# Optimization experiments

Measured on AMD Instinct MI355X. Metric: run time of the kernel, lower is better.

The kernel has to match this reference:

```python
import jax, jax.numpy as jnp
import numpy as np

N = 50000          # number of points
C = 64             # num_clusters (embedding width)
K_RAD = 32         # radius graph max_num_neighbors
K_KNN = 10         # knn graph k


def setup_inputs() -> dict:
    key = jax.random.key(0)
    ks = jax.random.split(key, 8)
    x0 = jax.random.normal(ks[0], (N, 3), jnp.float32)
    pos0 = jax.random.normal(ks[1], (N, 3), jnp.float32)
    # R0/t0 come from rigid_fitting in the original (external helper); use
    # orthonormal matrices from batched QR as realistic per-point rotations.
    A = jax.random.normal(ks[2], (N, 3, 3), jnp.float32)
    R0, _ = jnp.linalg.qr(A)
    t0 = jax.random.normal(ks[3], (N, 3), jnp.float32) * 0.1
    # pool1 k=1 assignment: point i -> cluster assign01[i]
    assign01 = jax.random.randint(ks[4], (N,), 0, C, dtype=jnp.int32)
    # radius graph edges (source, target): each point has K_RAD neighbors
    radius_src = jax.random.randint(ks[5], (N * K_RAD,), 0, N, dtype=jnp.int32)
    radius_dst = jnp.repeat(jnp.arange(N, dtype=jnp.int32), K_RAD)
    # knn-10 graph edges used by WeightedAvg
    knn_src = jax.random.randint(ks[6], (N * K_KNN,), 0, N, dtype=jnp.int32)
    knn_dst = jnp.repeat(jnp.arange(N, dtype=jnp.int32), K_KNN)
    return dict(x0=x0, pos0=pos0, R0=R0, t0=t0, assign01=assign01,
                radius_src=radius_src, radius_dst=radius_dst,
                knn_src=knn_src, knn_dst=knn_dst)


def _rigid_layer(xfeat, pos0, x0, R0, t0, src, dst):
    # RigidPropModule.message + max aggregation (nn=None, lin1: w=-1, b=0.01)
    Ri = R0[dst]                     # [E,3,3] target-side rotation
    ti = t0[dst]                     # [E,3]
    posj = pos0[src]                 # [E,3]
    xj = x0[src]                     # [E,3]
    pred = jnp.einsum('eij,ej->ei', Ri, posj) + ti
    d = jnp.sum((pred - xj) ** 2, axis=-1, keepdims=True)   # [E,1]
    w = jax.nn.sigmoid(-d + 0.01)
    msg = w * xfeat[src]             # [E,C]
    agg = jax.ops.segment_max(msg, dst, num_segments=xfeat.shape[0])
    # messages are non-negative; nodes with no edges get 0 (torch_scatter fill)
    return jnp.maximum(agg, 0.0)


def reference(x0, pos0, R0, t0, assign01, radius_src, radius_dst, knn_src, knn_dst):
    n = x0.shape[0]
    # scatter_add of one-hot cluster embeddings back to points
    emb = jnp.zeros((n, C), jnp.float32).at[jnp.arange(n), assign01].add(1.0)
    m1 = _rigid_layer(emb, pos0, x0, R0, t0, radius_src, radius_dst)
    m2 = _rigid_layer(m1, pos0, x0, R0, t0, radius_src, radius_dst)
    m3 = _rigid_layer(m2, pos0, x0, R0, t0, radius_src, radius_dst)
    m4 = _rigid_layer(m2, pos0, x0, R0, t0, radius_src, radius_dst)
    m5 = _rigid_layer(m2, pos0, x0, R0, t0, radius_src, radius_dst)
    msg = jnp.stack([m1.sum(-1), m2.sum(-1), m3.sum(-1),
                     m4.sum(-1), m5.sum(-1)], axis=-1)      # [N,5]
    # predictor: Linear(5,1) with w=ones, b=-17, then sigmoid
    conf = jax.nn.sigmoid(msg.sum(-1, keepdims=True) - 17.0)  # [N,1]
    # WeightedAvg over knn edges: out[t] = sum_s conf[s]*val[s] / sum_s conf[s]
    cw = conf[knn_src]                                       # [E,1]
    num_R = jax.ops.segment_sum(cw * R0.reshape(n, 9)[knn_src], knn_dst, num_segments=n)
    num_t = jax.ops.segment_sum(cw * t0[knn_src], knn_dst, num_segments=n)
    den = jax.ops.segment_sum(cw, knn_dst, num_segments=n) + 1e-8
    R_out = (num_R / den).reshape(n, 3, 3)
    t_out = num_t / den
    x_out = jnp.einsum('nij,nj->ni', R_out, pos0) + t_out
    return x_out, R_out, t_out
```

## Files before the change

kernel.cpp:

```cpp
#include <hip/hip_runtime.h>
#include <hip/hip_fp16.h>
#include <math.h>

#define N_PTS 50000
#define C_DIM 64
#define K_RAD 32
#define K_KNN 10
#define E_RAD (N_PTS * K_RAD)

__device__ inline __half2 hmax2(__half2 a, __half2 b) {
    __half2 d;
    asm("v_pk_max_f16 %0, %1, %2" : "=v"(d) : "v"(a), "v"(b));
    return d;
}

__device__ inline __half2 shfl_xor_h2(__half2 v, int mask) {
    int i = *(int*)&v;
    int r = __shfl_xor(i, mask);
    return *(__half2*)&r;
}

__global__ void pack_tables_kernel(const float* __restrict__ pos0,
                                   const float* __restrict__ x0,
                                   const int* __restrict__ assign,
                                   float4* __restrict__ geo) {
    int i = blockIdx.x * blockDim.x + threadIdx.x;
    if (i >= N_PTS) return;
    geo[i * 2 + 0] = make_float4(pos0[3 * i], pos0[3 * i + 1], pos0[3 * i + 2], x0[3 * i]);
    geo[i * 2 + 1] = make_float4(x0[3 * i + 1], x0[3 * i + 2], __int_as_float(assign[i]), 0.0f);
}

__global__ void ew_layer1_kernel(const float4* __restrict__ geo,
                                 const float* __restrict__ R0,
                                 const float* __restrict__ t0,
                                 const int* __restrict__ src,
                                 unsigned int* __restrict__ packed,
                                 __half* __restrict__ m1,
                                 float* __restrict__ sum1,
                                 float4* __restrict__ rt4) {
    __shared__ int lm[16][C_DIM];
    __shared__ float ldsR[16 * 9];
    __shared__ float ldsT[16 * 3];
    int tid = threadIdx.x;
    int blk = blockIdx.x;
    ((int*)lm)[tid] = 0;
    ((int*)lm)[tid + 256] = 0;
    ((int*)lm)[tid + 512] = 0;
    ((int*)lm)[tid + 768] = 0;
    if (tid < 144) ldsR[tid] = R0[blk * 144 + tid];
    if (tid < 48) ldsT[tid] = t0[blk * 48 + tid];
    int nl = tid >> 4;
    int ng = blk * 16 + nl;
    int e0 = tid & 15, e1 = e0 + 16;
    int s0 = src[ng * K_RAD + e0];
    int s1 = src[ng * K_RAD + e1];
    float4 g0a = geo[s0 * 2 + 0];
    float4 g0b = geo[s0 * 2 + 1];
    float4 g1a = geo[s1 * 2 + 0];
    float4 g1b = geo[s1 * 2 + 1];
    __syncthreads();
    if (tid < 48) {
        int n = tid / 3, slot = tid % 3;
        const float* R = ldsR + n * 9;
        const float* T = ldsT + n * 3;
        float4 q;
        if (slot == 0) q = make_float4(R[0], R[1], R[2], R[3]);
        else if (slot == 1) q = make_float4(R[4], R[5], R[6], R[7]);
        else q = make_float4(R[8], T[0], T[1], T[2]);
        rt4[(blk * 16 + n) * 4 + slot] = q;
    }
    const float* R = ldsR + nl * 9;
    const float* T = ldsT + nl * 3;
    float r0 = R[0] * g0a.x + R[1] * g0a.y + R[2] * g0a.z + T[0] - g0a.w;
    float r1 = R[3] * g0a.x + R[4] * g0a.y + R[5] * g0a.z + T[1] - g0b.x;
    float r2 = R[6] * g0a.x + R[7] * g0a.y + R[8] * g0a.z + T[2] - g0b.y;
    float d0 = r0 * r0 + r1 * r1 + r2 * r2;
    float w0 = 1.0f / (1.0f + __expf(d0 - 0.01f));
    float u0 = R[0] * g1a.x + R[1] * g1a.y + R[2] * g1a.z + T[0] - g1a.w;
    float u1 = R[3] * g1a.x + R[4] * g1a.y + R[5] * g1a.z + T[1] - g1b.x;
    float u2 = R[6] * g1a.x + R[7] * g1a.y + R[8] * g1a.z + T[2] - g1b.y;
    float d1 = u0 * u0 + u1 * u1 + u2 * u2;
    float w1 = 1.0f / (1.0f + __expf(d1 - 0.01f));
    packed[ng * K_RAD + e0] =
        ((unsigned int)s0 << 16) | (unsigned int)__half_as_ushort(__float2half_rn(w0));
    packed[ng * K_RAD + e1] =
        ((unsigned int)s1 << 16) | (unsigned int)__half_as_ushort(__float2half_rn(w1));
    atomicMax(&lm[nl][__float_as_int(g0b.z)], __float_as_int(w0));
    atomicMax(&lm[nl][__float_as_int(g1b.z)], __float_as_int(w1));
    __syncthreads();
    int c0 = (tid & 15) * 4;
    float v0 = __int_as_float(lm[nl][c0 + 0]);
    float v1 = __int_as_float(lm[nl][c0 + 1]);
    float v2 = __int_as_float(lm[nl][c0 + 2]);
    float v3 = __int_as_float(lm[nl][c0 + 3]);
    __half2 h01 = __floats2half2_rn(v0, v1);
    __half2 h23 = __floats2half2_rn(v2, v3);
    uint2 uo = make_uint2(*(unsigned int*)&h01, *(unsigned int*)&h23);
    *(uint2*)(m1 + ng * C_DIM + c0) = uo;
    float s = v0 + v1 + v2 + v3;
    s += __shfl_down(s, 8);
    s += __shfl_down(s, 4);
    s += __shfl_down(s, 2);
    s += __shfl_down(s, 1);
    if ((tid & 15) == 0) sum1[ng] = s;
}

__global__ void layer_pk_kernel(const unsigned int* __restrict__ packed,
                                const __half* __restrict__ xin,
                                __half* __restrict__ xout,
                                float* __restrict__ sum_out) {
    int gid = blockIdx.x * blockDim.x + threadIdx.x;
    int lane = gid & 63;
    int node = (gid >> 6) * 2 + (lane >> 5);
    int eslot = (lane >> 3) & 3;
    int cpos = lane & 7;
    const uint4* pk4 = (const uint4*)(packed + node * K_RAD + eslot * 8);
    uint4 q0 = pk4[0], q1 = pk4[1];
    unsigned int pes[8] = {q0.x, q0.y, q0.z, q0.w, q1.x, q1.y, q1.z, q1.w};
    __half2 a0 = __float2half2_rn(0.0f), a1 = a0, a2 = a0, a3 = a0;
#pragma unroll
    for (int p = 0; p < 8; ++p) {
        unsigned int pe = pes[p];
        float4 f = *(const float4*)(xin + (pe >> 16) * C_DIM + cpos * 8);
        __half2* h = (__half2*)&f;
        __half2 w2 = __half2half2(__ushort_as_half((unsigned short)(pe & 0xffffu)));
        a0 = hmax2(a0, __hmul2(w2, h[0]));
        a1 = hmax2(a1, __hmul2(w2, h[1]));
        a2 = hmax2(a2, __hmul2(w2, h[2]));
        a3 = hmax2(a3, __hmul2(w2, h[3]));
    }
#pragma unroll
    for (int off = 8; off <= 16; off <<= 1) {
        a0 = hmax2(a0, shfl_xor_h2(a0, off));
        a1 = hmax2(a1, shfl_xor_h2(a1, off));
        a2 = hmax2(a2, shfl_xor_h2(a2, off));
        a3 = hmax2(a3, shfl_xor_h2(a3, off));
    }
    if (eslot == 0) {
        float4 o;
        __half2* oh = (__half2*)&o;
        oh[0] = a0; oh[1] = a1; oh[2] = a2; oh[3] = a3;
        ((float4*)(xout + node * C_DIM))[cpos] = o;
    }
    float2 v0 = __half22float2(a0), v1 = __half22float2(a1);
    float2 v2 = __half22float2(a2), v3 = __half22float2(a3);
    float s = v0.x + v0.y + v1.x + v1.y + v2.x + v2.y + v3.x + v3.y;
    s += __shfl_xor(s, 1);
    s += __shfl_xor(s, 2);
    s += __shfl_xor(s, 4);
    if ((lane & 31) == 0) sum_out[node] = s;
}

__global__ void layer3_conf_pk_kernel(const unsigned int* __restrict__ packed,
                                      const __half* __restrict__ xin,
                                      const float* __restrict__ sum1,
                                      const float* __restrict__ sum2,
                                      float* __restrict__ rt4f) {
    int gid = blockIdx.x * blockDim.x + threadIdx.x;
    int lane = gid & 63;
    int node = (gid >> 6) * 2 + (lane >> 5);
    int eslot = (lane >> 3) & 3;
    int cpos = lane & 7;
    const uint4* pk4 = (const uint4*)(packed + node * K_RAD + eslot * 8);
    uint4 q0 = pk4[0], q1 = pk4[1];
    unsigned int pes[8] = {q0.x, q0.y, q0.z, q0.w, q1.x, q1.y, q1.z, q1.w};
    __half2 a0 = __float2half2_rn(0.0f), a1 = a0, a2 = a0, a3 = a0;
#pragma unroll
    for (int p = 0; p < 8; ++p) {
        unsigned int pe = pes[p];
        float4 f = *(const float4*)(xin + (pe >> 16) * C_DIM + cpos * 8);
        __half2* h = (__half2*)&f;
        __half2 w2 = __half2half2(__ushort_as_half((unsigned short)(pe & 0xffffu)));
        a0 = hmax2(a0, __hmul2(w2, h[0]));
        a1 = hmax2(a1, __hmul2(w2, h[1]));
        a2 = hmax2(a2, __hmul2(w2, h[2]));
        a3 = hmax2(a3, __hmul2(w2, h[3]));
    }
#pragma unroll
    for (int off = 8; off <= 16; off <<= 1) {
        a0 = hmax2(a0, shfl_xor_h2(a0, off));
        a1 = hmax2(a1, shfl_xor_h2(a1, off));
        a2 = hmax2(a2, shfl_xor_h2(a2, off));
        a3 = hmax2(a3, shfl_xor_h2(a3, off));
    }
    float2 v0 = __half22float2(a0), v1 = __half22float2(a1);
    float2 v2 = __half22float2(a2), v3 = __half22float2(a3);
    float s = v0.x + v0.y + v1.x + v1.y + v2.x + v2.y + v3.x + v3.y;
    s += __shfl_xor(s, 1);
    s += __shfl_xor(s, 2);
    s += __shfl_xor(s, 4);
    if ((lane & 31) == 0) {
        float tot = sum1[node] + sum2[node] + 3.0f * s - 17.0f;
        rt4f[node * 16 + 12] = 1.0f / (1.0f + __expf(-tot));
    }
}

__global__ void wavg_kernel(const int* __restrict__ knn_src,
                            const float4* __restrict__ rt4,
                            const float* __restrict__ pos0,
                            float* __restrict__ out) {
    int gid = blockIdx.x * blockDim.x + threadIdx.x;
    int lane = gid & 63;
    int t = (gid >> 6) * 16 + (lane >> 2);
    int part = lane & 3;
    if (t >= N_PTS) return;
    float4 acc = make_float4(0.f, 0.f, 0.f, 0.f);
    for (int j = 0; j < K_KNN; ++j) {
        int s = knn_src[t * K_KNN + j];
        float4 q = rt4[s * 4 + part];
        float c = __shfl(q.x, lane | 3);
        if (part == 3) {
            acc.x += c;
        } else {
            acc.x += c * q.x; acc.y += c * q.y;
            acc.z += c * q.z; acc.w += c * q.w;
        }
    }
    float den = __shfl(acc.x, lane | 3) + 1e-8f;
    float inv = 1.0f / den;
    float4 sc = make_float4(acc.x * inv, acc.y * inv, acc.z * inv, acc.w * inv);
    int base = lane & ~3;
    float R3 = __shfl(sc.w, base + 0);
    float R6 = __shfl(sc.z, base + 1);
    float R7 = __shfl(sc.w, base + 1);
    float t0v = __shfl(sc.y, base + 2);
    float t1v = __shfl(sc.z, base + 2);
    float px = pos0[t * 3 + 0], py = pos0[t * 3 + 1], pz = pos0[t * 3 + 2];
    float* Rout = out + N_PTS * 3;
    float* tout = out + N_PTS * 12;
    if (part == 0) {
        out[t * 3 + 0] = sc.x * px + sc.y * py + sc.z * pz + t0v;
        Rout[t * 9 + 0] = sc.x; Rout[t * 9 + 1] = sc.y;
        Rout[t * 9 + 2] = sc.z; Rout[t * 9 + 3] = sc.w;
    } else if (part == 1) {
        out[t * 3 + 1] = R3 * px + sc.x * py + sc.y * pz + t1v;
        Rout[t * 9 + 4] = sc.x; Rout[t * 9 + 5] = sc.y;
        Rout[t * 9 + 6] = sc.z; Rout[t * 9 + 7] = sc.w;
    } else if (part == 2) {
        out[t * 3 + 2] = R6 * px + R7 * py + sc.x * pz + sc.w;
        Rout[t * 9 + 8] = sc.x;
        tout[t * 3 + 0] = sc.y; tout[t * 3 + 1] = sc.z; tout[t * 3 + 2] = sc.w;
    }
}

extern "C" void kernel_launch(void* const* d_in, const int* in_sizes, int n_in,
                              void* d_out, int out_size, void* d_ws, size_t ws_size,
                              hipStream_t stream) {
    const float* x0 = (const float*)d_in[0];
    const float* pos0 = (const float*)d_in[1];
    const float* R0 = (const float*)d_in[2];
    const float* t0 = (const float*)d_in[3];
    const int* assign01 = (const int*)d_in[4];
    const int* radius_src = (const int*)d_in[5];
    const int* knn_src = (const int*)d_in[7];

    char* ws = (char*)d_ws;
    unsigned int* packed = (unsigned int*)ws;
    __half* mA = (__half*)(ws + 6400000);
    __half* mB = (__half*)(ws + 12800000);
    float4* geo = (float4*)(ws + 19200000);
    float4* rt4 = (float4*)(ws + 20800000);
    float* sum1 = (float*)(ws + 24000000);
    float* sum2 = (float*)(ws + 24200000);
    float* out = (float*)d_out;

    pack_tables_kernel<<<(N_PTS + 255) / 256, 256, 0, stream>>>(
        pos0, x0, assign01, geo);

    ew_layer1_kernel<<<N_PTS / 16, 256, 0, stream>>>(
        geo, R0, t0, radius_src, packed, mA, sum1, rt4);

    layer_pk_kernel<<<N_PTS / 8, 256, 0, stream>>>(
        packed, mA, mB, sum2);

    layer3_conf_pk_kernel<<<N_PTS / 8, 256, 0, stream>>>(
        packed, mB, sum1, sum2, (float*)rt4);

    wavg_kernel<<<(N_PTS * 4 + 255) / 256, 256, 0, stream>>>(
        knn_src, rt4, pos0, out);
}
```

Before: 136.4 us.

## Add nontemporal loads/stores, batch gathers, fold sums into rt4, split knn across lanes

Streaming index, packed-edge and output accesses now use nontemporal loads and stores so they do not pollute cache. In the two gather layers, all eight neighbor feature loads are issued before any compute, exposing more memory-level parallelism. The per-node layer sums are written into spare slots of the rt4 table instead of separate arrays. The weighted-average kernel splits each node's ten knn neighbors across two lane groups and combines them with a shuffle. These changes raise register use and double the wavg thread count.

```diff
diff --git a/kernel.cpp b/kernel.cpp
--- a/kernel.cpp
+++ b/kernel.cpp
@@ -6,7 +6,9 @@
 #define C_DIM 64
 #define K_RAD 32
 #define K_KNN 10
-#define E_RAD (N_PTS * K_RAD)
+
+typedef unsigned int uv4 __attribute__((ext_vector_type(4)));
+typedef unsigned int uv2 __attribute__((ext_vector_type(2)));
 
 __device__ inline __half2 hmax2(__half2 a, __half2 b) {
     __half2 d;
@@ -36,11 +38,11 @@
                                  const int* __restrict__ src,
                                  unsigned int* __restrict__ packed,
                                  __half* __restrict__ m1,
-                                 float* __restrict__ sum1,
                                  float4* __restrict__ rt4) {
     __shared__ int lm[16][C_DIM];
     __shared__ float ldsR[16 * 9];
     __shared__ float ldsT[16 * 3];
+    float* rt4f = (float*)rt4;
     int tid = threadIdx.x;
     int blk = blockIdx.x;
     ((int*)lm)[tid] = 0;
@@ -52,8 +54,8 @@
     int nl = tid >> 4;
     int ng = blk * 16 + nl;
     int e0 = tid & 15, e1 = e0 + 16;
-    int s0 = src[ng * K_RAD + e0];
-    int s1 = src[ng * K_RAD + e1];
+    int s0 = __builtin_nontemporal_load(src + ng * K_RAD + e0);
+    int s1 = __builtin_nontemporal_load(src + ng * K_RAD + e1);
     float4 g0a = geo[s0 * 2 + 0];
     float4 g0b = geo[s0 * 2 + 1];
     float4 g1a = geo[s1 * 2 + 0];
@@ -61,12 +63,12 @@
     __syncthreads();
     if (tid < 48) {
         int n = tid / 3, slot = tid % 3;
-        const float* R = ldsR + n * 9;
-        const float* T = ldsT + n * 3;
+        const float* Rp = ldsR + n * 9;
+        const float* Tp = ldsT + n * 3;
         float4 q;
-        if (slot == 0) q = make_float4(R[0], R[1], R[2], R[3]);
-        else if (slot == 1) q = make_float4(R[4], R[5], R[6], R[7]);
-        else q = make_float4(R[8], T[0], T[1], T[2]);
+        if (slot == 0) q = make_float4(Rp[0], Rp[1], Rp[2], Rp[3]);
+        else if (slot == 1) q = make_float4(Rp[4], Rp[5], Rp[6], Rp[7]);
+        else q = make_float4(Rp[8], Tp[0], Tp[1], Tp[2]);
         rt4[(blk * 16 + n) * 4 + slot] = q;
     }
     const float* R = ldsR + nl * 9;
@@ -81,10 +83,12 @@
     float u2 = R[6] * g1a.x + R[7] * g1a.y + R[8] * g1a.z + T[2] - g1b.y;
     float d1 = u0 * u0 + u1 * u1 + u2 * u2;
     float w1 = 1.0f / (1.0f + __expf(d1 - 0.01f));
-    packed[ng * K_RAD + e0] =
+    unsigned int p0 =
         ((unsigned int)s0 << 16) | (unsigned int)__half_as_ushort(__float2half_rn(w0));
-    packed[ng * K_RAD + e1] =
+    unsigned int p1 =
         ((unsigned int)s1 << 16) | (unsigned int)__half_as_ushort(__float2half_rn(w1));
+    __builtin_nontemporal_store(p0, packed + ng * K_RAD + e0);
+    __builtin_nontemporal_store(p1, packed + ng * K_RAD + e1);
     atomicMax(&lm[nl][__float_as_int(g0b.z)], __float_as_int(w0));
     atomicMax(&lm[nl][__float_as_int(g1b.z)], __float_as_int(w1));
     __syncthreads();
@@ -102,28 +106,31 @@
     s += __shfl_down(s, 4);
     s += __shfl_down(s, 2);
     s += __shfl_down(s, 1);
-    if ((tid & 15) == 0) sum1[ng] = s;
-}
-
-__global__ void layer_pk_kernel(const unsigned int* __restrict__ packed,
-                                const __half* __restrict__ xin,
-                                __half* __restrict__ xout,
-                                float* __restrict__ sum_out) {
+    if ((tid & 15) == 0) rt4f[ng * 16 + 12] = s - 17.0f;
+}
+
+__global__ void layer2_kernel(const unsigned int* __restrict__ packed,
+                              const __half* __restrict__ xin,
+                              __half* __restrict__ xout,
+                              float* __restrict__ rt4f) {
     int gid = blockIdx.x * blockDim.x + threadIdx.x;
     int lane = gid & 63;
     int node = (gid >> 6) * 2 + (lane >> 5);
     int eslot = (lane >> 3) & 3;
     int cpos = lane & 7;
-    const uint4* pk4 = (const uint4*)(packed + node * K_RAD + eslot * 8);
-    uint4 q0 = pk4[0], q1 = pk4[1];
+    const uv4* pk4 = (const uv4*)(packed + node * K_RAD + eslot * 8);
+    uv4 q0 = __builtin_nontemporal_load(pk4);
+    uv4 q1 = __builtin_nontemporal_load(pk4 + 1);
     unsigned int pes[8] = {q0.x, q0.y, q0.z, q0.w, q1.x, q1.y, q1.z, q1.w};
+    float4 f[8];
+#pragma unroll
+    for (int p = 0; p < 8; ++p)
+        f[p] = *(const float4*)(xin + (pes[p] >> 16) * C_DIM + cpos * 8);
     __half2 a0 = __float2half2_rn(0.0f), a1 = a0, a2 = a0, a3 = a0;
 #pragma unroll
     for (int p = 0; p < 8; ++p) {
-        unsigned int pe = pes[p];
-        float4 f = *(const float4*)(xin + (pe >> 16) * C_DIM + cpos * 8);
-        __half2* h = (__half2*)&f;
-        __half2 w2 = __half2half2(__ushort_as_half((unsigned short)(pe & 0xffffu)));
+        __half2* h = (__half2*)&f[p];
+        __half2 w2 = __half2half2(__ushort_as_half((unsigned short)(pes[p] & 0xffffu)));
         a0 = hmax2(a0, __hmul2(w2, h[0]));
         a1 = hmax2(a1, __hmul2(w2, h[1]));
         a2 = hmax2(a2, __hmul2(w2, h[2]));
@@ -148,29 +155,30 @@
     s += __shfl_xor(s, 1);
     s += __shfl_xor(s, 2);
     s += __shfl_xor(s, 4);
-    if ((lane & 31) == 0) sum_out[node] = s;
-}
-
-__global__ void layer3_conf_pk_kernel(const unsigned int* __restrict__ packed,
-                                      const __half* __restrict__ xin,
-                                      const float* __restrict__ sum1,
-                                      const float* __restrict__ sum2,
-                                      float* __restrict__ rt4f) {
+    if ((lane & 31) == 0) rt4f[node * 16 + 13] = s;
+}
+
+__global__ void layer3_conf_kernel(const unsigned int* __restrict__ packed,
+                                   const __half* __restrict__ xin,
+                                   float* __restrict__ rt4f) {
     int gid = blockIdx.x * blockDim.x + threadIdx.x;
     int lane = gid & 63;
     int node = (gid >> 6) * 2 + (lane >> 5);
     int eslot = (lane >> 3) & 3;
     int cpos = lane & 7;
-    const uint4* pk4 = (const uint4*)(packed + node * K_RAD + eslot * 8);
-    uint4 q0 = pk4[0], q1 = pk4[1];
+    const uv4* pk4 = (const uv4*)(packed + node * K_RAD + eslot * 8);
+    uv4 q0 = __builtin_nontemporal_load(pk4);
+    uv4 q1 = __builtin_nontemporal_load(pk4 + 1);
     unsigned int pes[8] = {q0.x, q0.y, q0.z, q0.w, q1.x, q1.y, q1.z, q1.w};
+    float4 f[8];
+#pragma unroll
+    for (int p = 0; p < 8; ++p)
+        f[p] = *(const float4*)(xin + (pes[p] >> 16) * C_DIM + cpos * 8);
     __half2 a0 = __float2half2_rn(0.0f), a1 = a0, a2 = a0, a3 = a0;
 #pragma unroll
     for (int p = 0; p < 8; ++p) {
-        unsigned int pe = pes[p];
-        float4 f = *(const float4*)(xin + (pe >> 16) * C_DIM + cpos * 8);
-        __half2* h = (__half2*)&f;
-        __half2 w2 = __half2half2(__ushort_as_half((unsigned short)(pe & 0xffffu)));
+        __half2* h = (__half2*)&f[p];
+        __half2 w2 = __half2half2(__ushort_as_half((unsigned short)(pes[p] & 0xffffu)));
         a0 = hmax2(a0, __hmul2(w2, h[0]));
         a1 = hmax2(a1, __hmul2(w2, h[1]));
         a2 = hmax2(a2, __hmul2(w2, h[2]));
@@ -190,7 +198,9 @@
     s += __shfl_xor(s, 2);
     s += __shfl_xor(s, 4);
     if ((lane & 31) == 0) {
-        float tot = sum1[node] + sum2[node] + 3.0f * s - 17.0f;
+        float base = rt4f[node * 16 + 12];
+        float s2 = rt4f[node * 16 + 13];
+        float tot = base + s2 + 3.0f * s;
         rt4f[node * 16 + 12] = 1.0f / (1.0f + __expf(-tot));
     }
 }
@@ -201,21 +211,32 @@
                             float* __restrict__ out) {
     int gid = blockIdx.x * blockDim.x + threadIdx.x;
     int lane = gid & 63;
-    int t = (gid >> 6) * 16 + (lane >> 2);
+    int t = gid >> 3;
     int part = lane & 3;
+    int half = (lane >> 2) & 1;
     if (t >= N_PTS) return;
+    int ids[5];
+#pragma unroll
+    for (int k = 0; k < 5; ++k)
+        ids[k] = __builtin_nontemporal_load(knn_src + t * K_KNN + half * 5 + k);
+    float4 q[5];
+#pragma unroll
+    for (int k = 0; k < 5; ++k) q[k] = rt4[ids[k] * 4 + part];
     float4 acc = make_float4(0.f, 0.f, 0.f, 0.f);
-    for (int j = 0; j < K_KNN; ++j) {
-        int s = knn_src[t * K_KNN + j];
-        float4 q = rt4[s * 4 + part];
-        float c = __shfl(q.x, lane | 3);
+#pragma unroll
+    for (int k = 0; k < 5; ++k) {
+        float c = __shfl(q[k].x, lane | 3);
         if (part == 3) {
             acc.x += c;
         } else {
-            acc.x += c * q.x; acc.y += c * q.y;
-            acc.z += c * q.z; acc.w += c * q.w;
+            acc.x += c * q[k].x; acc.y += c * q[k].y;
+            acc.z += c * q[k].z; acc.w += c * q[k].w;
         }
     }
+    acc.x += __shfl_xor(acc.x, 4);
+    acc.y += __shfl_xor(acc.y, 4);
+    acc.z += __shfl_xor(acc.z, 4);
+    acc.w += __shfl_xor(acc.w, 4);
     float den = __shfl(acc.x, lane | 3) + 1e-8f;
     float inv = 1.0f / den;
     float4 sc = make_float4(acc.x * inv, acc.y * inv, acc.z * inv, acc.w * inv);
@@ -225,21 +246,29 @@
     float R7 = __shfl(sc.w, base + 1);
     float t0v = __shfl(sc.y, base + 2);
     float t1v = __shfl(sc.z, base + 2);
-    float px = pos0[t * 3 + 0], py = pos0[t * 3 + 1], pz = pos0[t * 3 + 2];
-    float* Rout = out + N_PTS * 3;
-    float* tout = out + N_PTS * 12;
-    if (part == 0) {
-        out[t * 3 + 0] = sc.x * px + sc.y * py + sc.z * pz + t0v;
-        Rout[t * 9 + 0] = sc.x; Rout[t * 9 + 1] = sc.y;
-        Rout[t * 9 + 2] = sc.z; Rout[t * 9 + 3] = sc.w;
-    } else if (part == 1) {
-        out[t * 3 + 1] = R3 * px + sc.x * py + sc.y * pz + t1v;
-        Rout[t * 9 + 4] = sc.x; Rout[t * 9 + 5] = sc.y;
-        Rout[t * 9 + 6] = sc.z; Rout[t * 9 + 7] = sc.w;
-    } else if (part == 2) {
-        out[t * 3 + 2] = R6 * px + R7 * py + sc.x * pz + sc.w;
-        Rout[t * 9 + 8] = sc.x;
-        tout[t * 3 + 0] = sc.y; tout[t * 3 + 1] = sc.z; tout[t * 3 + 2] = sc.w;
+    if (half == 0) {
+        float px = pos0[t * 3 + 0], py = pos0[t * 3 + 1], pz = pos0[t * 3 + 2];
+        float* Rout = out + N_PTS * 3;
+        float* tout = out + N_PTS * 12;
+        if (part == 0) {
+            __builtin_nontemporal_store(sc.x * px + sc.y * py + sc.z * pz + t0v, out + t * 3 + 0);
+            __builtin_nontemporal_store(sc.x, Rout + t * 9 + 0);
+            __builtin_nontemporal_store(sc.y, Rout + t * 9 + 1);
+            __builtin_nontemporal_store(sc.z, Rout + t * 9 + 2);
+            __builtin_nontemporal_store(sc.w, Rout + t * 9 + 3);
+        } else if (part == 1) {
+            __builtin_nontemporal_store(R3 * px + sc.x * py + sc.y * pz + t1v, out + t * 3 + 1);
+            __builtin_nontemporal_store(sc.x, Rout + t * 9 + 4);
+            __builtin_nontemporal_store(sc.y, Rout + t * 9 + 5);
+            __builtin_nontemporal_store(sc.z, Rout + t * 9 + 6);
+            __builtin_nontemporal_store(sc.w, Rout + t * 9 + 7);
+        } else if (part == 2) {
+            __builtin_nontemporal_store(R6 * px + R7 * py + sc.x * pz + sc.w, out + t * 3 + 2);
+            __builtin_nontemporal_store(sc.x, Rout + t * 9 + 8);
+            __builtin_nontemporal_store(sc.y, tout + t * 3 + 0);
+            __builtin_nontemporal_store(sc.z, tout + t * 3 + 1);
+            __builtin_nontemporal_store(sc.w, tout + t * 3 + 2);
+        }
     }
 }
 
@@ -260,22 +289,20 @@
     __half* mB = (__half*)(ws + 12800000);
     float4* geo = (float4*)(ws + 19200000);
     float4* rt4 = (float4*)(ws + 20800000);
-    float* sum1 = (float*)(ws + 24000000);
-    float* sum2 = (float*)(ws + 24200000);
     float* out = (float*)d_out;
 
     pack_tables_kernel<<<(N_PTS + 255) / 256, 256, 0, stream>>>(
         pos0, x0, assign01, geo);
 
     ew_layer1_kernel<<<N_PTS / 16, 256, 0, stream>>>(
-        geo, R0, t0, radius_src, packed, mA, sum1, rt4);
-
-    layer_pk_kernel<<<N_PTS / 8, 256, 0, stream>>>(
-        packed, mA, mB, sum2);
-
-    layer3_conf_pk_kernel<<<N_PTS / 8, 256, 0, stream>>>(
-        packed, mB, sum1, sum2, (float*)rt4);
-
-    wavg_kernel<<<(N_PTS * 4 + 255) / 256, 256, 0, stream>>>(
+        geo, R0, t0, radius_src, packed, mA, rt4);
+
+    layer2_kernel<<<N_PTS / 8, 256, 0, stream>>>(
+        packed, mA, mB, (float*)rt4);
+
+    layer3_conf_kernel<<<N_PTS / 8, 256, 0, stream>>>(
+        packed, mB, (float*)rt4);
+
+    wavg_kernel<<<(N_PTS * 8 + 255) / 256, 256, 0, stream>>>(
         knn_src, rt4, pos0, out);
 }
```

New measurement: 138.2 us. No clear change (+1.3%).
